# Kernel tuning notes

Measured on AMD Instinct MI355X. Metric: run time of the kernel, lower is better.

Reference implementation:

```python
import jax, jax.numpy as jnp
import numpy as np

ALPHA = 0.2  # LeakyReLU negative slope


def gat_layer(x, W, a, alpha=ALPHA):
    """Multi-head dense GAT layer.
    x: (B, N, F); W: (H, F, O); a: (H, 2*O, 1).
    Returns (B, N, H*O) — ELU(head outputs) concatenated over heads.
    """
    H, F, O = W.shape
    Wh = jnp.einsum('bnf,hfo->bhno', x, W)          # (B,H,N,O)
    a_src = a[:, :O, 0]                              # (H,O)
    a_dst = a[:, O:, 0]                              # (H,O)
    s_src = jnp.einsum('bhno,ho->bhn', Wh, a_src)    # (B,H,N)
    s_dst = jnp.einsum('bhno,ho->bhn', Wh, a_dst)    # (B,H,N)
    e = s_src[..., :, None] + s_dst[..., None, :]    # (B,H,N,N)
    e = jax.nn.leaky_relu(e, negative_slope=alpha)
    att = jax.nn.softmax(e, axis=-1)                 # softmax over neighbors j
    out = jnp.einsum('bhnm,bhmo->bhno', att, Wh)     # (B,H,N,O)
    out = jax.nn.elu(out)
    B, _, N, _ = out.shape
    return jnp.transpose(out, (0, 2, 1, 3)).reshape(B, N, H * O)


def setup_inputs() -> dict:
    key = jax.random.key(0)
    ks = jax.random.split(key, 5)
    B, N = 32, 1024
    x = jax.random.normal(ks[0], (B, N, 4), dtype=jnp.float32)
    # layer1: nfeat=4, nhid=2, nheads=3
    W1 = jax.random.normal(ks[1], (3, 4, 2), dtype=jnp.float32) * 0.5
    a1 = jax.random.normal(ks[2], (3, 4, 1), dtype=jnp.float32) * 0.5
    # layer2: nfeat=6, nhid=4, nheads=1
    W2 = jax.random.normal(ks[3], (1, 6, 4), dtype=jnp.float32) * 0.5
    a2 = jax.random.normal(ks[4], (1, 8, 1), dtype=jnp.float32) * 0.5
    return {"x": x, "W1": W1, "a1": a1, "W2": W2, "a2": a2}


def reference(x, W1, a1, W2, a2):
    h = gat_layer(x, W1, a1)   # (B, N, 6)
    y = gat_layer(h, W2, a2)   # (B, N, 4)
    return y
```

## Files before the change

kernel.cpp:

```cpp
#include <hip/hip_runtime.h>


#define GAT_ALPHA 0.2f
#define LOG2E 1.44269504088896f

__device__ __forceinline__ float ex2(float v) { return __builtin_amdgcn_exp2f(v); }

template <int F, int O, int H>
__global__ __launch_bounds__(256) void gat_bucket_kernel(
    const float* __restrict__ x,
    const float* __restrict__ Wt,
    const float* __restrict__ at,
    float* __restrict__ out)
{
    constexpr int N = 1024, NT = 256, EPT = N / NT;
    constexpr int NB = 512;
    constexpr int A1 = O + 1;

    const int bid   = blockIdx.x;
    const int h     = bid % H;
    const int b     = bid / H;
    const int tid   = threadIdx.x;
    const int wv    = tid >> 6, ln = tid & 63;

    float Wl[F][O], asrc[O], adst[O];
#pragma unroll
    for (int f = 0; f < F; ++f)
#pragma unroll
        for (int o = 0; o < O; ++o) Wl[f][o] = Wt[(h * F + f) * O + o];
#pragma unroll
    for (int o = 0; o < O; ++o) {
        asrc[o] = at[h * 2 * O + o];
        adst[o] = at[h * 2 * O + O + o];
    }

    __shared__ float sSrc[N];
    __shared__ int   sCS[NB + 1];
    __shared__ float sKey[N];
    __shared__ float sWhS[O][N];
    __shared__ float sPre[A1][NB + 1];
    __shared__ float sSuf[A1][NB + 1];
    __shared__ float sMM[8];
    __shared__ int   sRedI[4];
    __shared__ float sRedF[2][A1][4];

    for (int i = tid; i < NB + 1; i += NT) sCS[i] = 0;
    for (int i = tid; i < A1 * (NB + 1); i += NT) {
        (&sPre[0][0])[i] = 0.0f;
        (&sSuf[0][0])[i] = 0.0f;
    }

    float key[EPT], wh[EPT][O];
    float kmin = 3.4e38f, kmax = -3.4e38f;
    const float* xb = x + (size_t)b * N * F;
#pragma unroll
    for (int k = 0; k < EPT; ++k) {
        const int m = k * NT + tid;
        float xv[F];
        if constexpr (F == 4) {
            const float4 v = ((const float4*)xb)[m];
            xv[0] = v.x; xv[1] = v.y; xv[2] = v.z; xv[3] = v.w;
        } else {
            const float2* x2 = (const float2*)xb;
            const float2 va = x2[3 * m], vb = x2[3 * m + 1], vc = x2[3 * m + 2];
            xv[0] = va.x; xv[1] = va.y; xv[2] = vb.x;
            xv[3] = vb.y; xv[4] = vc.x; xv[5] = vc.y;
        }
        float d = 0.0f, sn = 0.0f;
#pragma unroll
        for (int o = 0; o < O; ++o) {
            float acc = 0.0f;
#pragma unroll
            for (int f = 0; f < F; ++f) acc += xv[f] * Wl[f][o];
            wh[k][o] = acc;
            d += acc * adst[o];
            sn += acc * asrc[o];
        }
        key[k] = d;
        sSrc[m] = sn;
        kmin = fminf(kmin, d);
        kmax = fmaxf(kmax, d);
    }
#pragma unroll
    for (int s = 1; s < 64; s <<= 1) {
        kmin = fminf(kmin, __shfl_xor(kmin, s, 64));
        kmax = fmaxf(kmax, __shfl_xor(kmax, s, 64));
    }
    if (ln == 0) { sMM[wv] = kmin; sMM[4 + wv] = kmax; }
    __syncthreads();

    kmin = fminf(fminf(sMM[0], sMM[1]), fminf(sMM[2], sMM[3]));
    kmax = fmaxf(fmaxf(sMM[4], sMM[5]), fmaxf(sMM[6], sMM[7]));
    const float invw = (float)NB / fmaxf(kmax - kmin, 1e-30f);

    int bk[EPT], rk[EPT];
#pragma unroll
    for (int k = 0; k < EPT; ++k) {
        int q = (int)((key[k] - kmin) * invw);
        q = q < 0 ? 0 : (q > NB - 1 ? NB - 1 : q);
        bk[k] = q;
        rk[k] = atomicAdd(&sCS[q], 1);
        const float e1 = ex2(LOG2E * key[k]);
        const float e2 = ex2(GAT_ALPHA * LOG2E * key[k]);
        atomicAdd(&sSuf[0][q], e1);
        atomicAdd(&sPre[0][q], e2);
#pragma unroll
        for (int o = 0; o < O; ++o) {
            atomicAdd(&sSuf[1 + o][q], e1 * wh[k][o]);
            atomicAdd(&sPre[1 + o][q], e2 * wh[k][o]);
        }
    }
    __syncthreads();

    const int c0 = sCS[2 * tid], c1 = sCS[2 * tid + 1];
    float p0[A1], p1[A1], s0[A1], s1[A1];
#pragma unroll
    for (int a = 0; a < A1; ++a) {
        p0[a] = sPre[a][2 * tid]; p1[a] = sPre[a][2 * tid + 1];
        s0[a] = sSuf[a][2 * tid]; s1[a] = sSuf[a][2 * tid + 1];
    }
    int irun = c0 + c1;
#pragma unroll
    for (int s = 1; s < 64; s <<= 1) {
        const int u = __shfl_up(irun, s, 64);
        if (ln >= s) irun += u;
    }
    if (ln == 63) sRedI[wv] = irun;
    int irex = __shfl_up(irun, 1, 64);
    if (ln == 0) irex = 0;

    float prun[A1], prex[A1], srun[A1], srex[A1];
#pragma unroll
    for (int a = 0; a < A1; ++a) {
        prun[a] = p0[a] + p1[a];
#pragma unroll
        for (int s = 1; s < 64; s <<= 1) {
            const float u = __shfl_up(prun[a], s, 64);
            if (ln >= s) prun[a] += u;
        }
        if (ln == 63) sRedF[0][a][wv] = prun[a];
        prex[a] = __shfl_up(prun[a], 1, 64);
        if (ln == 0) prex[a] = 0.0f;

        srun[a] = s0[a] + s1[a];
#pragma unroll
        for (int s = 1; s < 64; s <<= 1) {
            const float u = __shfl_down(srun[a], s, 64);
            if (ln < 64 - s) srun[a] += u;
        }
        if (ln == 0) sRedF[1][a][wv] = srun[a];
        srex[a] = __shfl_down(srun[a], 1, 64);
        if (ln == 63) srex[a] = 0.0f;
    }
    __syncthreads();

    {
        int ibase = 0;
        for (int w = 0; w < 4; ++w) if (w < wv) ibase += sRedI[w];
        const int iex = ibase + irex;
        sCS[2 * tid] = iex;
        sCS[2 * tid + 1] = iex + c0;
        if (tid == 0) sCS[NB] = N;
    }
#pragma unroll
    for (int a = 0; a < A1; ++a) {
        float pbase = 0.0f, sbase = 0.0f;
        for (int w = 0; w < 4; ++w) {
            if (w < wv) pbase += sRedF[0][a][w];
            if (w > wv) sbase += sRedF[1][a][w];
        }
        const float pex = pbase + prex[a];
        sPre[a][2 * tid] = pex;
        sPre[a][2 * tid + 1] = pex + p0[a];
        const float sex = sbase + srex[a];
        sSuf[a][2 * tid + 1] = sex + s1[a];
        sSuf[a][2 * tid] = sex + s1[a] + s0[a];
    }
    __syncthreads();

#pragma unroll
    for (int k = 0; k < EPT; ++k) {
        const int pos = sCS[bk[k]] + rk[k];
        sKey[pos] = key[k];
#pragma unroll
        for (int o = 0; o < O; ++o) sWhS[o][pos] = wh[k][o];
    }
    __syncthreads();

    for (int rr = tid; rr < N; rr += NT) {
        const int row = rr;
        const float sn = sSrc[row];
        const float rho = ex2(0.8f * LOG2E * sn);
        int bq = (int)((-sn - kmin) * invw);
        bq = bq < 0 ? 0 : (bq > NB - 1 ? NB - 1 : bq);
        const int i0 = sCS[bq], i1 = sCS[bq + 1];
        float den = rho * sSuf[0][bq + 1] + sPre[0][bq];
        float num[O];
#pragma unroll
        for (int o = 0; o < O; ++o)
            num[o] = rho * sSuf[1 + o][bq + 1] + sPre[1 + o][bq];
        for (int i = i0; i < i1; ++i) {
            const float kk = sKey[i];
            const float w = fmaxf(rho * ex2(LOG2E * kk), ex2(GAT_ALPHA * LOG2E * kk));
            den += w;
#pragma unroll
            for (int o = 0; o < O; ++o) num[o] += w * sWhS[o][i];
        }
#pragma unroll
        for (int o = 0; o < O; ++o) {
            float v = num[o] / den;
            v = (v > 0.0f) ? v : (__expf(v) - 1.0f);
            out[((size_t)b * N + row) * (H * O) + h * O + o] = v;
        }
    }
}

extern "C" void kernel_launch(void* const* d_in, const int* in_sizes, int n_in,
                              void* d_out, int out_size, void* d_ws, size_t ws_size,
                              hipStream_t stream) {
    const float* x  = (const float*)d_in[0];
    const float* W1 = (const float*)d_in[1];
    const float* a1 = (const float*)d_in[2];
    const float* W2 = (const float*)d_in[3];
    const float* a2 = (const float*)d_in[4];

    float* h1 = (float*)d_ws;
    float* y  = (float*)d_out;

    constexpr int B = 32;
    gat_bucket_kernel<4, 2, 3><<<B * 3, 256, 0, stream>>>(x, W1, a1, h1);
    gat_bucket_kernel<6, 4, 1><<<B * 1, 256, 0, stream>>>(h1, W2, a2, y);
}
```

Baseline: 97.40 us.

## Use 1024-thread blocks and assign each prefix-scan array to its own wavefront

Raises the block size from 256 to 1024 threads, so each thread handles one node instead of four and the per-row attention loop runs one row per thread. The block-wide multi-array scan is replaced by independent single-wavefront scans: one wave scans the bucket counts, others scan each prefix array and each suffix array over 8 buckets per lane. This drops a barrier and the cross-wave combine step, and exposes more parallelism for the small grids (96 and 32 blocks). The cost is heavier shared-memory atomic contention per block, larger register pressure limits at 1024 threads, and the scan phase now uses only up to 11 of 16 waves.

After: 91.51 us. 6.0% less time.

```diff
diff --git a/kernel.cpp b/kernel.cpp
--- a/kernel.cpp
+++ b/kernel.cpp
@@ -6,22 +6,25 @@
 
 __device__ __forceinline__ float ex2(float v) { return __builtin_amdgcn_exp2f(v); }
 
-template <int F, int O, int H>
-__global__ __launch_bounds__(256) void gat_bucket_kernel(
+template <int F, int O, int H, int NT>
+__global__ __launch_bounds__(NT) void gat_bucket_kernel(
     const float* __restrict__ x,
     const float* __restrict__ Wt,
     const float* __restrict__ at,
     float* __restrict__ out)
 {
-    constexpr int N = 1024, NT = 256, EPT = N / NT;
+    constexpr int N = 1024, EPT = N / NT;
     constexpr int NB = 512;
     constexpr int A1 = O + 1;
-
-    const int bid   = blockIdx.x;
-    const int h     = bid % H;
-    const int b     = bid / H;
-    const int tid   = threadIdx.x;
-    const int wv    = tid >> 6, ln = tid & 63;
+    constexpr int NW = NT / 64;
+    constexpr int NJOBS = 2 * A1 + 1;
+    constexpr int BPL = NB / 64;
+
+    const int bid = blockIdx.x;
+    const int h   = bid % H;
+    const int b   = bid / H;
+    const int tid = threadIdx.x;
+    const int wv  = tid >> 6, ln = tid & 63;
 
     float Wl[F][O], asrc[O], adst[O];
 #pragma unroll
@@ -40,9 +43,7 @@
     __shared__ float sWhS[O][N];
     __shared__ float sPre[A1][NB + 1];
     __shared__ float sSuf[A1][NB + 1];
-    __shared__ float sMM[8];
-    __shared__ int   sRedI[4];
-    __shared__ float sRedF[2][A1][4];
+    __shared__ float sMM[2 * NW];
 
     for (int i = tid; i < NB + 1; i += NT) sCS[i] = 0;
     for (int i = tid; i < A1 * (NB + 1); i += NT) {
@@ -86,11 +87,15 @@
         kmin = fminf(kmin, __shfl_xor(kmin, s, 64));
         kmax = fmaxf(kmax, __shfl_xor(kmax, s, 64));
     }
-    if (ln == 0) { sMM[wv] = kmin; sMM[4 + wv] = kmax; }
-    __syncthreads();
-
-    kmin = fminf(fminf(sMM[0], sMM[1]), fminf(sMM[2], sMM[3]));
-    kmax = fmaxf(fmaxf(sMM[4], sMM[5]), fmaxf(sMM[6], sMM[7]));
+    if (ln == 0) { sMM[wv] = kmin; sMM[NW + wv] = kmax; }
+    __syncthreads();
+
+    kmin = sMM[0]; kmax = sMM[NW];
+#pragma unroll
+    for (int w = 1; w < NW; ++w) {
+        kmin = fminf(kmin, sMM[w]);
+        kmax = fmaxf(kmax, sMM[NW + w]);
+    }
     const float invw = (float)NB / fmaxf(kmax - kmin, 1e-30f);
 
     int bk[EPT], rk[EPT];
@@ -112,69 +117,68 @@
     }
     __syncthreads();
 
-    const int c0 = sCS[2 * tid], c1 = sCS[2 * tid + 1];
-    float p0[A1], p1[A1], s0[A1], s1[A1];
-#pragma unroll
-    for (int a = 0; a < A1; ++a) {
-        p0[a] = sPre[a][2 * tid]; p1[a] = sPre[a][2 * tid + 1];
-        s0[a] = sSuf[a][2 * tid]; s1[a] = sSuf[a][2 * tid + 1];
-    }
-    int irun = c0 + c1;
-#pragma unroll
-    for (int s = 1; s < 64; s <<= 1) {
-        const int u = __shfl_up(irun, s, 64);
-        if (ln >= s) irun += u;
-    }
-    if (ln == 63) sRedI[wv] = irun;
-    int irex = __shfl_up(irun, 1, 64);
-    if (ln == 0) irex = 0;
-
-    float prun[A1], prex[A1], srun[A1], srex[A1];
-#pragma unroll
-    for (int a = 0; a < A1; ++a) {
-        prun[a] = p0[a] + p1[a];
-#pragma unroll
-        for (int s = 1; s < 64; s <<= 1) {
-            const float u = __shfl_up(prun[a], s, 64);
-            if (ln >= s) prun[a] += u;
-        }
-        if (ln == 63) sRedF[0][a][wv] = prun[a];
-        prex[a] = __shfl_up(prun[a], 1, 64);
-        if (ln == 0) prex[a] = 0.0f;
-
-        srun[a] = s0[a] + s1[a];
-#pragma unroll
-        for (int s = 1; s < 64; s <<= 1) {
-            const float u = __shfl_down(srun[a], s, 64);
-            if (ln < 64 - s) srun[a] += u;
-        }
-        if (ln == 0) sRedF[1][a][wv] = srun[a];
-        srex[a] = __shfl_down(srun[a], 1, 64);
-        if (ln == 63) srex[a] = 0.0f;
-    }
-    __syncthreads();
-
-    {
-        int ibase = 0;
-        for (int w = 0; w < 4; ++w) if (w < wv) ibase += sRedI[w];
-        const int iex = ibase + irex;
-        sCS[2 * tid] = iex;
-        sCS[2 * tid + 1] = iex + c0;
-        if (tid == 0) sCS[NB] = N;
-    }
-#pragma unroll
-    for (int a = 0; a < A1; ++a) {
-        float pbase = 0.0f, sbase = 0.0f;
-        for (int w = 0; w < 4; ++w) {
-            if (w < wv) pbase += sRedF[0][a][w];
-            if (w > wv) sbase += sRedF[1][a][w];
-        }
-        const float pex = pbase + prex[a];
-        sPre[a][2 * tid] = pex;
-        sPre[a][2 * tid + 1] = pex + p0[a];
-        const float sex = sbase + srex[a];
-        sSuf[a][2 * tid + 1] = sex + s1[a];
-        sSuf[a][2 * tid] = sex + s1[a] + s0[a];
+    if (wv < NJOBS) {
+        if (wv == 0) {
+            int c[BPL];
+#pragma unroll
+            for (int i = 0; i < BPL; ++i) c[i] = sCS[ln * BPL + i];
+            int s = 0;
+#pragma unroll
+            for (int i = 0; i < BPL; ++i) s += c[i];
+            int run = s;
+#pragma unroll
+            for (int d = 1; d < 64; d <<= 1) {
+                const int u = __shfl_up(run, d, 64);
+                if (ln >= d) run += u;
+            }
+            int acc = run - s;
+#pragma unroll
+            for (int i = 0; i < BPL; ++i) {
+                const int t = acc; acc += c[i];
+                sCS[ln * BPL + i] = t;
+            }
+            if (ln == 0) sCS[NB] = N;
+        } else if (wv <= A1) {
+            float* arr = &sPre[wv - 1][0];
+            float v[BPL];
+#pragma unroll
+            for (int i = 0; i < BPL; ++i) v[i] = arr[ln * BPL + i];
+            float s = 0.0f;
+#pragma unroll
+            for (int i = 0; i < BPL; ++i) s += v[i];
+            float run = s;
+#pragma unroll
+            for (int d = 1; d < 64; d <<= 1) {
+                const float u = __shfl_up(run, d, 64);
+                if (ln >= d) run += u;
+            }
+            float acc = run - s;
+#pragma unroll
+            for (int i = 0; i < BPL; ++i) {
+                const float t = acc; acc += v[i];
+                arr[ln * BPL + i] = t;
+            }
+        } else {
+            float* arr = &sSuf[wv - A1 - 1][0];
+            float v[BPL];
+#pragma unroll
+            for (int i = 0; i < BPL; ++i) v[i] = arr[ln * BPL + i];
+            float s = 0.0f;
+#pragma unroll
+            for (int i = 0; i < BPL; ++i) s += v[i];
+            float run = s;
+#pragma unroll
+            for (int d = 1; d < 64; d <<= 1) {
+                const float u = __shfl_down(run, d, 64);
+                if (ln < 64 - d) run += u;
+            }
+            float acc = run - s;
+#pragma unroll
+            for (int i = BPL - 1; i >= 0; --i) {
+                acc += v[i];
+                arr[ln * BPL + i] = acc;
+            }
+        }
     }
     __syncthreads();
 
@@ -188,8 +192,7 @@
     __syncthreads();
 
     for (int rr = tid; rr < N; rr += NT) {
-        const int row = rr;
-        const float sn = sSrc[row];
+        const float sn = sSrc[rr];
         const float rho = ex2(0.8f * LOG2E * sn);
         int bq = (int)((-sn - kmin) * invw);
         bq = bq < 0 ? 0 : (bq > NB - 1 ? NB - 1 : bq);
@@ -210,7 +213,7 @@
         for (int o = 0; o < O; ++o) {
             float v = num[o] / den;
             v = (v > 0.0f) ? v : (__expf(v) - 1.0f);
-            out[((size_t)b * N + row) * (H * O) + h * O + o] = v;
+            out[((size_t)b * N + rr) * (H * O) + h * O + o] = v;
         }
     }
 }
@@ -228,6 +231,6 @@
     float* y  = (float*)d_out;
 
     constexpr int B = 32;
-    gat_bucket_kernel<4, 2, 3><<<B * 3, 256, 0, stream>>>(x, W1, a1, h1);
-    gat_bucket_kernel<6, 4, 1><<<B * 1, 256, 0, stream>>>(h1, W2, a2, y);
+    gat_bucket_kernel<4, 2, 3, 1024><<<B * 3, 1024, 0, stream>>>(x, W1, a1, h1);
+    gat_bucket_kernel<6, 4, 1, 1024><<<B * 1, 1024, 0, stream>>>(h1, W2, a2, y);
 }
```
